# Performance work log

Measured on AMD Instinct MI355X. Metric: run time of the kernel, lower is better.

## Reference

```python
import jax, jax.numpy as jnp
import numpy as np

DIM = 2048
NUM_HEADS = 16
HEAD_DIM = DIM // NUM_HEADS
SCALE = 1.0 / np.sqrt(HEAD_DIM)


def setup_inputs() -> dict:
    key = jax.random.key(0)
    ks = jax.random.split(key, 5)
    B, S = 2, 2048
    w_std = 1.0 / np.sqrt(DIM)
    return {
        "hidden_states": jax.random.normal(ks[0], (B, S, DIM), dtype=jnp.float32),
        "Wq": jax.random.normal(ks[1], (DIM, DIM), dtype=jnp.float32) * w_std,
        "Wk": jax.random.normal(ks[2], (DIM, DIM), dtype=jnp.float32) * w_std,
        "Wv": jax.random.normal(ks[3], (DIM, DIM), dtype=jnp.float32) * w_std,
        "Wo": jax.random.normal(ks[4], (DIM, DIM), dtype=jnp.float32) * w_std,
    }


def reference(hidden_states, Wq, Wk, Wv, Wo):
    B, S, _ = hidden_states.shape
    # nn.Linear(dim, dim, bias=False): y = x @ W.T
    q = (hidden_states @ Wq.T).reshape(B, S, NUM_HEADS, HEAD_DIM)
    k = (hidden_states @ Wk.T).reshape(B, S, NUM_HEADS, HEAD_DIM)
    v = (hidden_states @ Wv.T).reshape(B, S, NUM_HEADS, HEAD_DIM)
    # Causal softmax attention (equivalent to the module's blockwise
    # online-softmax _efficient_attention, dropout = 0).
    scores = jnp.einsum("bqhd,bkhd->bhqk", q, k) * SCALE
    causal = jnp.tril(jnp.ones((S, S), dtype=bool))  # [S,S], True = keep
    scores = jnp.where(causal[None, None, :, :], scores, -jnp.inf)
    attn = jax.nn.softmax(scores, axis=-1)
    out = jnp.einsum("bhqk,bkhd->bqhd", attn, v).reshape(B, S, DIM)
    return out @ Wo.T
```

## Files before the change

### kernel.cpp

```cpp
#include <hip/hip_runtime.h>
#include <cmath>

typedef _Float16 f16x8 __attribute__((ext_vector_type(8)));
typedef _Float16 f16x4 __attribute__((ext_vector_type(4)));
typedef float    f32x4 __attribute__((ext_vector_type(4)));

#define LOG2E 1.4426950408889634f

__device__ __forceinline__ void load_lds16(const void* g, void* l) {
  __builtin_amdgcn_global_load_lds(
      (const __attribute__((address_space(1))) unsigned int*)g,
      (__attribute__((address_space(3))) unsigned int*)l, 16, 0, 0);
}

__global__ __launch_bounds__(256) void cvt_f32_f16(const float* __restrict__ in,
                                                   _Float16* __restrict__ out,
                                                   int n4) {
  int i = blockIdx.x * blockDim.x + threadIdx.x;
  int stride = gridDim.x * blockDim.x;
  for (; i < n4; i += stride) {
    float4 v = ((const float4*)in)[i];
    f16x4 h = { (_Float16)v.x, (_Float16)v.y, (_Float16)v.z, (_Float16)v.w };
    ((f16x4*)out)[i] = h;
  }
}

__global__ __launch_bounds__(256) void cvt_w4(const float* __restrict__ w0,
                                              const float* __restrict__ w1,
                                              const float* __restrict__ w2,
                                              const float* __restrict__ w3,
                                              _Float16* __restrict__ o0,
                                              _Float16* __restrict__ o1,
                                              _Float16* __restrict__ o2,
                                              _Float16* __restrict__ o3,
                                              int n4) {
  const float* in = (blockIdx.y == 0) ? w0 : (blockIdx.y == 1) ? w1
                  : (blockIdx.y == 2) ? w2 : w3;
  _Float16* out = (blockIdx.y == 0) ? o0 : (blockIdx.y == 1) ? o1
                : (blockIdx.y == 2) ? o2 : o3;
  int i = blockIdx.x * blockDim.x + threadIdx.x;
  int stride = gridDim.x * blockDim.x;
  for (; i < n4; i += stride) {
    float4 v = ((const float4*)in)[i];
    f16x4 h = { (_Float16)v.x, (_Float16)v.y, (_Float16)v.z, (_Float16)v.w };
    ((f16x4*)out)[i] = h;
  }
}

__device__ __forceinline__ void gemm_core(const _Float16* __restrict__ A,
                                          const _Float16* __restrict__ B,
                                          _Float16* Asm, _Float16* Bsm,
                                          f32x4 acc[4][4]) {
  const int tid  = threadIdx.x;
  const int wave = tid >> 6, lane = tid & 63;
  const int g = lane >> 4, l15 = lane & 15;
  const int wm = wave >> 1, wn = wave & 1;
  const int srow = tid >> 2, sslot = tid & 3;

  const _Float16* Abase = A + (size_t)(blockIdx.x * 128) * 2048;
  const _Float16* Bbase = B + (size_t)(blockIdx.y * 128) * 2048;

  for (int k0 = 0; k0 < 2048; k0 += 32) {
#pragma unroll
    for (int i = 0; i < 2; ++i) {
      int row = i * 64 + srow;
      int sp  = sslot ^ ((row >> 1) & 3);
      load_lds16(Abase + (size_t)row * 2048 + k0 + sp * 8,
                 (char*)Asm + i * 4096 + wave * 1024);
      load_lds16(Bbase + (size_t)row * 2048 + k0 + sp * 8,
                 (char*)Bsm + i * 4096 + wave * 1024);
    }
    __syncthreads();

    f16x8 af[4], bf[4];
#pragma unroll
    for (int mi = 0; mi < 4; ++mi) {
      int row = wm * 64 + mi * 16 + l15;
      af[mi] = *(const f16x8*)((const char*)Asm + row * 64 +
                               ((g ^ ((row >> 1) & 3)) << 4));
    }
#pragma unroll
    for (int ni = 0; ni < 4; ++ni) {
      int row = wn * 64 + ni * 16 + l15;
      bf[ni] = *(const f16x8*)((const char*)Bsm + row * 64 +
                               ((g ^ ((row >> 1) & 3)) << 4));
    }
#pragma unroll
    for (int mi = 0; mi < 4; ++mi)
#pragma unroll
      for (int ni = 0; ni < 4; ++ni)
        acc[mi][ni] = __builtin_amdgcn_mfma_f32_16x16x32_f16(af[mi], bf[ni],
                                                             acc[mi][ni], 0, 0, 0);
    __syncthreads();
  }
}

__global__ __launch_bounds__(256) void gemm_qkv(
    const _Float16* __restrict__ Xh,
    const _Float16* __restrict__ Wq, const _Float16* __restrict__ Wk,
    const _Float16* __restrict__ Wv,
    _Float16* __restrict__ Qb, _Float16* __restrict__ Kb,
    _Float16* __restrict__ Vt, float qscale) {
  __shared__ _Float16 Asm[128 * 32], Bsm[128 * 32];
  const int z = blockIdx.z;
  const _Float16* B = (z == 0) ? Wq : (z == 1) ? Wk : Wv;
  f32x4 acc[4][4] = {};
  gemm_core(Xh, B, Asm, Bsm, acc);

  const int tid = threadIdx.x;
  const int wave = tid >> 6, lane = tid & 63;
  const int g = lane >> 4, l15 = lane & 15;
  const int wm = wave >> 1, wn = wave & 1;
  const float scale = (z == 0) ? qscale : 1.0f;
#pragma unroll
  for (int mi = 0; mi < 4; ++mi)
#pragma unroll
    for (int ni = 0; ni < 4; ++ni)
#pragma unroll
      for (int r = 0; r < 4; ++r) {
        int row = blockIdx.x * 128 + wm * 64 + mi * 16 + g * 4 + r;
        int col = blockIdx.y * 128 + wn * 64 + ni * 16 + l15;
        float v = acc[mi][ni][r] * scale;
        int b = row >> 11, sq = row & 2047, h = col >> 7, d = col & 127;
        if (z < 2) {
          _Float16* dst = (z == 0) ? Qb : Kb;
          dst[(((size_t)b * 16 + h) * 2048 + sq) * 128 + d] = (_Float16)v;
        } else {
          Vt[(((size_t)b * 16 + h) * 128 + d) * 2048 + sq] = (_Float16)v;
        }
      }
}

__global__ __launch_bounds__(256) void gemm_out(
    const _Float16* __restrict__ AO, const _Float16* __restrict__ Wo,
    float* __restrict__ C) {
  __shared__ _Float16 Asm[128 * 32], Bsm[128 * 32];
  f32x4 acc[4][4] = {};
  gemm_core(AO, Wo, Asm, Bsm, acc);

  const int tid = threadIdx.x;
  const int wave = tid >> 6, lane = tid & 63;
  const int g = lane >> 4, l15 = lane & 15;
  const int wm = wave >> 1, wn = wave & 1;
#pragma unroll
  for (int mi = 0; mi < 4; ++mi)
#pragma unroll
    for (int ni = 0; ni < 4; ++ni)
#pragma unroll
      for (int r = 0; r < 4; ++r) {
        int row = blockIdx.x * 128 + wm * 64 + mi * 16 + g * 4 + r;
        int col = blockIdx.y * 128 + wn * 64 + ni * 16 + l15;
        C[(size_t)row * 2048 + col] = acc[mi][ni][r];
      }
}

__global__ __launch_bounds__(256, 2) void attn_fwd(
    const _Float16* __restrict__ Qb, const _Float16* __restrict__ Kb,
    const _Float16* __restrict__ Vt, _Float16* __restrict__ AO) {
  const int id  = blockIdx.x;
  const int xcd = id & 7, j = id >> 3;
  const int bh  = xcd * 4 + (j & 3);
  const int qb  = 15 - (j >> 2);

  const int tid = threadIdx.x;
  const int wave = tid >> 6, lane = tid & 63;
  const int g = lane >> 4, l15 = lane & 15;

  __shared__ _Float16 Ksm[2][64 * 128];
  __shared__ _Float16 Vsm[2][64 * 128];
  __shared__ _Float16 Psm[4][32 * 64];

  const _Float16* qp =
      Qb + ((size_t)bh * 2048 + qb * 128 + wave * 32 + l15) * 128;
  f16x8 qf[2][4];
#pragma unroll
  for (int mi = 0; mi < 2; ++mi)
#pragma unroll
    for (int c = 0; c < 4; ++c)
      qf[mi][c] = *(const f16x8*)(qp + mi * 16 * 128 + c * 32 + g * 8);

  f32x4 po[2][8] = {};
  float m[2][4], lsum[2][4];
#pragma unroll
  for (int mi = 0; mi < 2; ++mi)
#pragma unroll
    for (int r = 0; r < 4; ++r) { m[mi][r] = -1e30f; lsum[mi][r] = 0.f; }

  char* Pb = (char*)&Psm[wave][0];
  const int NT  = 2 * qb + 2;
  const int NTw = 2 * qb + 1 + (wave >> 1);
  const int dt  = 2 * qb + (wave >> 1);

  const int k_i  = tid >> 4, k_sp = (tid & 15) ^ (tid >> 4);
  const int v_i  = tid >> 3, v_sp = (tid & 7) ^ ((tid >> 3) & 7);
  const _Float16* kbase = Kb + (size_t)bh * 2048 * 128;
  const _Float16* vbase = Vt + (size_t)bh * 128 * 2048;

  auto stage = [&](int buf, int t) {
    char* kdst = (char*)&Ksm[buf][0] + wave * 1024;
    char* vdst = (char*)&Vsm[buf][0] + wave * 1024;
    const _Float16* kb = kbase + (size_t)t * 64 * 128;
    const _Float16* vb = vbase + t * 64;
#pragma unroll
    for (int i = 0; i < 4; ++i) {
      load_lds16(kb + (size_t)(i * 16 + k_i) * 128 + k_sp * 8, kdst + i * 4096);
      load_lds16(vb + (size_t)(i * 32 + v_i) * 2048 + v_sp * 8, vdst + i * 4096);
    }
  };

  stage(0, 0);
  __syncthreads();

  int buf = 0;
  for (int t = 0; t < NT; ++t) {
    if (t + 1 < NT) stage(buf ^ 1, t + 1);

    if (t < NTw) {
      const char* Kl = (const char*)&Ksm[buf][0];
      const char* Vl = (const char*)&Vsm[buf][0];

      f32x4 s[2][4];
      __builtin_amdgcn_s_setprio(1);
#pragma unroll
      for (int n = 0; n < 4; ++n) {
        f32x4 a0 = {0.f, 0.f, 0.f, 0.f}, a1 = {0.f, 0.f, 0.f, 0.f};
#pragma unroll
        for (int c = 0; c < 4; ++c) {
          int slot = (c * 4 + g) ^ l15;
          f16x8 kf = *(const f16x8*)(Kl + (n * 16 + l15) * 256 + (slot << 4));
          a0 = __builtin_amdgcn_mfma_f32_16x16x32_f16(qf[0][c], kf, a0, 0, 0, 0);
          a1 = __builtin_amdgcn_mfma_f32_16x16x32_f16(qf[1][c], kf, a1, 0, 0, 0);
        }
        s[0][n] = a0; s[1][n] = a1;
      }
      __builtin_amdgcn_s_setprio(0);

      if (t == dt) {
#pragma unroll
        for (int mi = 0; mi < 2; ++mi)
#pragma unroll
          for (int n = 0; n < 4; ++n)
#pragma unroll
            for (int r = 0; r < 4; ++r) {
              int key = t * 64 + n * 16 + l15;
              int qr  = qb * 128 + wave * 32 + mi * 16 + g * 4 + r;
              if (key > qr) s[mi][n][r] = -1e30f;
            }
      }

#pragma unroll
      for (int mi = 0; mi < 2; ++mi)
#pragma unroll
        for (int r = 0; r < 4; ++r) {
          float mx = fmaxf(fmaxf(s[mi][0][r], s[mi][1][r]),
                           fmaxf(s[mi][2][r], s[mi][3][r]));
#pragma unroll
          for (int off = 1; off < 16; off <<= 1) mx = fmaxf(mx, __shfl_xor(mx, off));
          float mn = fmaxf(m[mi][r], mx);
          float sc = exp2f(m[mi][r] - mn);
          m[mi][r] = mn;
          float rs = 0.f;
#pragma unroll
          for (int n = 0; n < 4; ++n) {
            float p = exp2f(s[mi][n][r] - mn);
            s[mi][n][r] = p;
            rs += p;
          }
#pragma unroll
          for (int off = 1; off < 16; off <<= 1) rs += __shfl_xor(rs, off);
          lsum[mi][r] = lsum[mi][r] * sc + rs;
#pragma unroll
          for (int no = 0; no < 8; ++no) po[mi][no][r] *= sc;
        }

#pragma unroll
      for (int mi = 0; mi < 2; ++mi)
#pragma unroll
        for (int n = 0; n < 4; ++n)
#pragma unroll
          for (int r = 0; r < 4; ++r) {
            int row = mi * 16 + g * 4 + r, key = n * 16 + l15;
            *(_Float16*)(Pb + row * 128 + (((key >> 3) ^ (row & 7)) << 4) +
                         (key & 7) * 2) = (_Float16)s[mi][n][r];
          }

      f16x8 pf[2][2];
#pragma unroll
      for (int mi = 0; mi < 2; ++mi)
#pragma unroll
        for (int kc = 0; kc < 2; ++kc) {
          int slot = (kc * 4 + g) ^ (l15 & 7);
          pf[mi][kc] = *(const f16x8*)(Pb + (mi * 16 + l15) * 128 + (slot << 4));
        }
      __builtin_amdgcn_s_setprio(1);
#pragma unroll
      for (int no = 0; no < 8; ++no)
#pragma unroll
        for (int kc = 0; kc < 2; ++kc) {
          int vrow = no * 16 + l15;
          int slot = (kc * 4 + g) ^ (l15 & 7);
          f16x8 vf = *(const f16x8*)(Vl + vrow * 128 + (slot << 4));
          po[0][no] = __builtin_amdgcn_mfma_f32_16x16x32_f16(pf[0][kc], vf,
                                                             po[0][no], 0, 0, 0);
          po[1][no] = __builtin_amdgcn_mfma_f32_16x16x32_f16(pf[1][kc], vf,
                                                             po[1][no], 0, 0, 0);
        }
      __builtin_amdgcn_s_setprio(0);
    }

    __syncthreads();
    buf ^= 1;
  }

  const int b = bh >> 4, h = bh & 15;
#pragma unroll
  for (int mi = 0; mi < 2; ++mi)
#pragma unroll
    for (int r = 0; r < 4; ++r) {
      float inv = 1.0f / lsum[mi][r];
      size_t row = (size_t)b * 2048 + qb * 128 + wave * 32 + mi * 16 + g * 4 + r;
#pragma unroll
      for (int no = 0; no < 8; ++no) {
        int col = h * 128 + no * 16 + l15;
        AO[row * 2048 + col] = (_Float16)(po[mi][no][r] * inv);
      }
    }
}

extern "C" void kernel_launch(void* const* d_in, const int* in_sizes, int n_in,
                              void* d_out, int out_size, void* d_ws, size_t ws_size,
                              hipStream_t stream) {
  const float* X  = (const float*)d_in[0];
  const float* Wq = (const float*)d_in[1];
  const float* Wk = (const float*)d_in[2];
  const float* Wv = (const float*)d_in[3];
  const float* Wo = (const float*)d_in[4];
  float* out = (float*)d_out;

  char* ws = (char*)d_ws;
  _Float16* Xh  = (_Float16*)(ws);
  _Float16* Wqh = (_Float16*)(ws + (16u << 20));
  _Float16* Wkh = (_Float16*)(ws + (24u << 20));
  _Float16* Wvh = (_Float16*)(ws + (32u << 20));
  _Float16* Woh = (_Float16*)(ws + (40u << 20));
  _Float16* Qb  = (_Float16*)(ws + (48u << 20));
  _Float16* Kb  = (_Float16*)(ws + (64u << 20));
  _Float16* Vt  = (_Float16*)(ws + (80u << 20));
  _Float16* AO  = (_Float16*)(ws + (96u << 20));

  cvt_f32_f16<<<2048, 256, 0, stream>>>(X, Xh, 8388608 / 4);
  cvt_w4<<<dim3(512, 4), 256, 0, stream>>>(Wq, Wk, Wv, Wo, Wqh, Wkh, Wvh, Woh,
                                           4194304 / 4);

  const float qscale = LOG2E / sqrtf(128.0f);
  gemm_qkv<<<dim3(32, 16, 3), 256, 0, stream>>>(Xh, Wqh, Wkh, Wvh, Qb, Kb, Vt, qscale);
  attn_fwd<<<512, 256, 0, stream>>>(Qb, Kb, Vt, AO);
  gemm_out<<<dim3(32, 16), 256, 0, stream>>>(AO, Woh, out);
}
```

Measured before the change: 451.0 us.

## Double-buffer GEMM LDS tiles to overlap global loads with MFMA

The shared GEMM core now uses two LDS buffers per operand, issuing the direct-to-LDS loads for the next K-slice before computing on the current one. This removes one barrier per iteration and is meant to hide global-load latency behind the MFMA work. It also raises wave priority around the MFMA block. LDS usage per block doubles to 32 KB, which may reduce occupancy. Correctness depends on the async global_load_lds completing before the single trailing barrier.

```diff
diff --git a/kernel.cpp b/kernel.cpp
--- a/kernel.cpp
+++ b/kernel.cpp
@@ -60,38 +60,49 @@
   const _Float16* Abase = A + (size_t)(blockIdx.x * 128) * 2048;
   const _Float16* Bbase = B + (size_t)(blockIdx.y * 128) * 2048;
 
+  const int r0 = srow, r1 = srow + 64;
+  const int sp0 = sslot ^ ((r0 >> 1) & 3);
+  const int sp1 = sslot ^ ((r1 >> 1) & 3);
+
+  auto stage = [&](int buf, int k0) {
+    char* Ad = (char*)Asm + buf * 8192 + wave * 1024;
+    char* Bd = (char*)Bsm + buf * 8192 + wave * 1024;
+    load_lds16(Abase + (size_t)r0 * 2048 + k0 + sp0 * 8, Ad);
+    load_lds16(Abase + (size_t)r1 * 2048 + k0 + sp1 * 8, Ad + 4096);
+    load_lds16(Bbase + (size_t)r0 * 2048 + k0 + sp0 * 8, Bd);
+    load_lds16(Bbase + (size_t)r1 * 2048 + k0 + sp1 * 8, Bd + 4096);
+  };
+
+  stage(0, 0);
+  __syncthreads();
+
+  int buf = 0;
   for (int k0 = 0; k0 < 2048; k0 += 32) {
-#pragma unroll
-    for (int i = 0; i < 2; ++i) {
-      int row = i * 64 + srow;
-      int sp  = sslot ^ ((row >> 1) & 3);
-      load_lds16(Abase + (size_t)row * 2048 + k0 + sp * 8,
-                 (char*)Asm + i * 4096 + wave * 1024);
-      load_lds16(Bbase + (size_t)row * 2048 + k0 + sp * 8,
-                 (char*)Bsm + i * 4096 + wave * 1024);
-    }
-    __syncthreads();
-
+    if (k0 + 32 < 2048) stage(buf ^ 1, k0 + 32);
+
+    const char* Ab = (const char*)Asm + buf * 8192;
+    const char* Bb = (const char*)Bsm + buf * 8192;
     f16x8 af[4], bf[4];
 #pragma unroll
     for (int mi = 0; mi < 4; ++mi) {
       int row = wm * 64 + mi * 16 + l15;
-      af[mi] = *(const f16x8*)((const char*)Asm + row * 64 +
-                               ((g ^ ((row >> 1) & 3)) << 4));
+      af[mi] = *(const f16x8*)(Ab + row * 64 + ((g ^ ((row >> 1) & 3)) << 4));
     }
 #pragma unroll
     for (int ni = 0; ni < 4; ++ni) {
       int row = wn * 64 + ni * 16 + l15;
-      bf[ni] = *(const f16x8*)((const char*)Bsm + row * 64 +
-                               ((g ^ ((row >> 1) & 3)) << 4));
-    }
+      bf[ni] = *(const f16x8*)(Bb + row * 64 + ((g ^ ((row >> 1) & 3)) << 4));
+    }
+    __builtin_amdgcn_s_setprio(1);
 #pragma unroll
     for (int mi = 0; mi < 4; ++mi)
 #pragma unroll
       for (int ni = 0; ni < 4; ++ni)
         acc[mi][ni] = __builtin_amdgcn_mfma_f32_16x16x32_f16(af[mi], bf[ni],
                                                              acc[mi][ni], 0, 0, 0);
+    __builtin_amdgcn_s_setprio(0);
     __syncthreads();
+    buf ^= 1;
   }
 }
 
@@ -101,7 +112,7 @@
     const _Float16* __restrict__ Wv,
     _Float16* __restrict__ Qb, _Float16* __restrict__ Kb,
     _Float16* __restrict__ Vt, float qscale) {
-  __shared__ _Float16 Asm[128 * 32], Bsm[128 * 32];
+  __shared__ _Float16 Asm[2 * 128 * 32], Bsm[2 * 128 * 32];
   const int z = blockIdx.z;
   const _Float16* B = (z == 0) ? Wq : (z == 1) ? Wk : Wv;
   f32x4 acc[4][4] = {};
@@ -134,7 +145,7 @@
 __global__ __launch_bounds__(256) void gemm_out(
     const _Float16* __restrict__ AO, const _Float16* __restrict__ Wo,
     float* __restrict__ C) {
-  __shared__ _Float16 Asm[128 * 32], Bsm[128 * 32];
+  __shared__ _Float16 Asm[2 * 128 * 32], Bsm[2 * 128 * 32];
   f32x4 acc[4][4] = {};
   gemm_core(AO, Wo, Asm, Bsm, acc);
 
```

Result: no change. 451.7 us (+0.1%).

## Rewrite QKV projection GEMM as 256x256 tiled, double-buffered 8-wave kernel

Applied to the files above, without the earlier changes.

Replaces the 128x128 single-buffered QKV GEMM with a 256x256 tile kernel using 512 threads (8 waves), double-buffered LDS staged through direct global-to-LDS loads. Prefetch of the next K tile is interleaved with MFMA phases, with explicit vmcnt waits, barriers and setprio. The aim is more operand reuse per load and hiding global memory latency behind compute. The cost is more LDS (128KB per block), fewer blocks (384), and a hand-managed wait/barrier protocol that is easy to get subtly wrong.

```diff
diff --git a/kernel.cpp b/kernel.cpp
--- a/kernel.cpp
+++ b/kernel.cpp
@@ -47,6 +47,129 @@
   }
 }
 
+__global__ __launch_bounds__(512, 2) void gemm_qkv_8p(
+    const _Float16* __restrict__ Xh,
+    const _Float16* __restrict__ Wq, const _Float16* __restrict__ Wk,
+    const _Float16* __restrict__ Wv,
+    _Float16* __restrict__ Qb, _Float16* __restrict__ Kb,
+    _Float16* __restrict__ Vt, float qscale) {
+  __shared__ _Float16 Asm[2][2][256][32];
+  __shared__ _Float16 Bsm[2][2][256][32];
+
+  const int tid = threadIdx.x;
+  const int wave = tid >> 6, lane = tid & 63;
+  const int g = lane >> 4, l15 = lane & 15;
+  const int wm = wave >> 2, wn = wave & 3;
+  const int z = blockIdx.z;
+  const _Float16* Bw = (z == 0) ? Wq : (z == 1) ? Wk : Wv;
+  const _Float16* Ab = Xh + (size_t)(blockIdx.x * 256) * 2048;
+  const _Float16* Bb = Bw + (size_t)(blockIdx.y * 256) * 2048;
+
+  const int r0 = tid >> 2, r1 = r0 + 128;
+  const int g0 = (tid & 3) ^ ((r0 >> 2) & 3);
+  const int g1 = (tid & 3) ^ ((r1 >> 2) & 3);
+  const size_t o0 = (size_t)r0 * 2048 + g0 * 8;
+  const size_t o1 = (size_t)r1 * 2048 + g1 * 8;
+
+  auto stageA = [&](int buf, int kh, int k0) {
+    char* d = (char*)Asm + (size_t)(buf * 2 + kh) * 16384 + wave * 1024;
+    load_lds16(Ab + o0 + k0 + kh * 32, d);
+    load_lds16(Ab + o1 + k0 + kh * 32, d + 8192);
+  };
+  auto stageB = [&](int buf, int kh, int k0) {
+    char* d = (char*)Bsm + (size_t)(buf * 2 + kh) * 16384 + wave * 1024;
+    load_lds16(Bb + o0 + k0 + kh * 32, d);
+    load_lds16(Bb + o1 + k0 + kh * 32, d + 8192);
+  };
+
+  f32x4 acc[8][4] = {};
+
+  stageA(0, 0, 0); stageB(0, 0, 0);
+  stageA(0, 1, 0); stageB(0, 1, 0);
+
+  const int NT = 32;
+#pragma unroll 2
+  for (int t = 0; t < NT; ++t) {
+    const int buf = t & 1;
+    const int k0n = (t + 1) * 64;
+    const bool pf = (t + 1 < NT);
+#pragma unroll
+    for (int kh = 0; kh < 2; ++kh) {
+      if (pf || kh == 0)
+        asm volatile("s_waitcnt vmcnt(4)" ::: "memory");
+      else
+        asm volatile("s_waitcnt vmcnt(0)" ::: "memory");
+      __builtin_amdgcn_s_barrier();
+      asm volatile("" ::: "memory");
+
+      const char* Al = (const char*)Asm + (size_t)(buf * 2 + kh) * 16384;
+      const char* Bl = (const char*)Bsm + (size_t)(buf * 2 + kh) * 16384;
+
+      f16x8 bfr[4];
+#pragma unroll
+      for (int cf = 0; cf < 4; ++cf) {
+        int c = wn * 64 + cf * 16 + l15;
+        bfr[cf] = *(const f16x8*)(Bl + c * 64 + ((g ^ ((c >> 2) & 3)) << 4));
+      }
+      {
+        f16x8 af[4];
+#pragma unroll
+        for (int j = 0; j < 4; ++j) {
+          int r = wm * 128 + j * 16 + l15;
+          af[j] = *(const f16x8*)(Al + r * 64 + ((g ^ ((r >> 2) & 3)) << 4));
+        }
+        if (pf) stageA(buf ^ 1, kh, k0n);
+        __builtin_amdgcn_s_setprio(1);
+#pragma unroll
+        for (int j = 0; j < 4; ++j)
+#pragma unroll
+          for (int cf = 0; cf < 4; ++cf)
+            acc[j][cf] = __builtin_amdgcn_mfma_f32_16x16x32_f16(
+                af[j], bfr[cf], acc[j][cf], 0, 0, 0);
+        __builtin_amdgcn_s_setprio(0);
+      }
+      __builtin_amdgcn_s_barrier();
+      asm volatile("" ::: "memory");
+      {
+        f16x8 af[4];
+#pragma unroll
+        for (int j = 0; j < 4; ++j) {
+          int r = wm * 128 + (4 + j) * 16 + l15;
+          af[j] = *(const f16x8*)(Al + r * 64 + ((g ^ ((r >> 2) & 3)) << 4));
+        }
+        if (pf) stageB(buf ^ 1, kh, k0n);
+        __builtin_amdgcn_s_setprio(1);
+#pragma unroll
+        for (int j = 0; j < 4; ++j)
+#pragma unroll
+          for (int cf = 0; cf < 4; ++cf)
+            acc[4 + j][cf] = __builtin_amdgcn_mfma_f32_16x16x32_f16(
+                af[j], bfr[cf], acc[4 + j][cf], 0, 0, 0);
+        __builtin_amdgcn_s_setprio(0);
+      }
+    }
+  }
+
+  const float scale = (z == 0) ? qscale : 1.0f;
+#pragma unroll
+  for (int rf = 0; rf < 8; ++rf)
+#pragma unroll
+    for (int cf = 0; cf < 4; ++cf)
+#pragma unroll
+      for (int rr = 0; rr < 4; ++rr) {
+        int row = blockIdx.x * 256 + wm * 128 + rf * 16 + g * 4 + rr;
+        int col = blockIdx.y * 256 + wn * 64 + cf * 16 + l15;
+        float v = acc[rf][cf][rr] * scale;
+        int b = row >> 11, sq = row & 2047, h = col >> 7, d = col & 127;
+        if (z < 2) {
+          _Float16* dst = (z == 0) ? Qb : Kb;
+          dst[(((size_t)b * 16 + h) * 2048 + sq) * 128 + d] = (_Float16)v;
+        } else {
+          Vt[(((size_t)b * 16 + h) * 128 + d) * 2048 + sq] = (_Float16)v;
+        }
+      }
+}
+
 __device__ __forceinline__ void gemm_core(const _Float16* __restrict__ A,
                                           const _Float16* __restrict__ B,
                                           _Float16* Asm, _Float16* Bsm,
@@ -93,42 +216,6 @@
                                                              acc[mi][ni], 0, 0, 0);
     __syncthreads();
   }
-}
-
-__global__ __launch_bounds__(256) void gemm_qkv(
-    const _Float16* __restrict__ Xh,
-    const _Float16* __restrict__ Wq, const _Float16* __restrict__ Wk,
-    const _Float16* __restrict__ Wv,
-    _Float16* __restrict__ Qb, _Float16* __restrict__ Kb,
-    _Float16* __restrict__ Vt, float qscale) {
-  __shared__ _Float16 Asm[128 * 32], Bsm[128 * 32];
-  const int z = blockIdx.z;
-  const _Float16* B = (z == 0) ? Wq : (z == 1) ? Wk : Wv;
-  f32x4 acc[4][4] = {};
-  gemm_core(Xh, B, Asm, Bsm, acc);
-
-  const int tid = threadIdx.x;
-  const int wave = tid >> 6, lane = tid & 63;
-  const int g = lane >> 4, l15 = lane & 15;
-  const int wm = wave >> 1, wn = wave & 1;
-  const float scale = (z == 0) ? qscale : 1.0f;
-#pragma unroll
-  for (int mi = 0; mi < 4; ++mi)
-#pragma unroll
-    for (int ni = 0; ni < 4; ++ni)
-#pragma unroll
-      for (int r = 0; r < 4; ++r) {
-        int row = blockIdx.x * 128 + wm * 64 + mi * 16 + g * 4 + r;
-        int col = blockIdx.y * 128 + wn * 64 + ni * 16 + l15;
-        float v = acc[mi][ni][r] * scale;
-        int b = row >> 11, sq = row & 2047, h = col >> 7, d = col & 127;
-        if (z < 2) {
-          _Float16* dst = (z == 0) ? Qb : Kb;
-          dst[(((size_t)b * 16 + h) * 2048 + sq) * 128 + d] = (_Float16)v;
-        } else {
-          Vt[(((size_t)b * 16 + h) * 128 + d) * 2048 + sq] = (_Float16)v;
-        }
-      }
 }
 
 __global__ __launch_bounds__(256) void gemm_out(
@@ -353,7 +440,8 @@
                                            4194304 / 4);
 
   const float qscale = LOG2E / sqrtf(128.0f);
-  gemm_qkv<<<dim3(32, 16, 3), 256, 0, stream>>>(Xh, Wqh, Wkh, Wvh, Qb, Kb, Vt, qscale);
+  gemm_qkv_8p<<<dim3(16, 8, 3), 512, 0, stream>>>(Xh, Wqh, Wkh, Wvh, Qb, Kb, Vt,
+                                                  qscale);
   attn_fwd<<<512, 256, 0, stream>>>(Qb, Kb, Vt, AO);
   gemm_out<<<dim3(32, 16), 256, 0, stream>>>(AO, Woh, out);
 }
```

Result: slower. 471.0 us (+4.4%).
